# Kernel optimization log

Measured on AMD Instinct MI355X. Metric: run time of the kernel, lower is better.

Reference implementation:

```python
import jax, jax.numpy as jnp
import numpy as np

N_QUBITS = 10
Q_DEPTH = 6
MAX_LAYERS = 15
DIM = 2 ** N_QUBITS
INV_SQRT2 = 0.7071067811865476

# PennyLane ordering: wire 0 is the most-significant bit of the state index.
# All gates (H, RY, CNOT) are real, so the state stays real float32.

def _split(state, wire):
    a = 2 ** wire
    b = 2 ** (N_QUBITS - wire - 1)
    return state.reshape(-1, a, 2, b)

def apply_h(state, wire):
    s = _split(state, wire)
    s0, s1 = s[:, :, 0], s[:, :, 1]
    out = jnp.stack([(s0 + s1) * INV_SQRT2, (s0 - s1) * INV_SQRT2], axis=2)
    return out.reshape(-1, DIM)

def apply_ry(state, theta, wire):
    # theta: scalar (shared weight) or (B,) per-sample angle
    c = jnp.cos(theta * 0.5).reshape(-1, 1, 1)
    sn = jnp.sin(theta * 0.5).reshape(-1, 1, 1)
    s = _split(state, wire)
    s0, s1 = s[:, :, 0], s[:, :, 1]
    out = jnp.stack([c * s0 - sn * s1, sn * s0 + c * s1], axis=2)
    return out.reshape(-1, DIM)

def apply_cnot(state, ctrl):
    # CNOT on adjacent wires [ctrl, ctrl+1]
    a = 2 ** ctrl
    b = 2 ** (N_QUBITS - ctrl - 2)
    s = state.reshape(-1, a, 2, 2, b)
    out = jnp.stack([s[:, :, 0], s[:, :, 1, ::-1]], axis=2)
    return out.reshape(-1, DIM)

def expval_z(state):
    # <Z_j> = P(qubit j = 0) - P(qubit j = 1)
    zs = []
    for w in range(N_QUBITS):
        s = _split(state, w)
        p = s * s
        zs.append(jnp.sum(p[:, :, 0], axis=(1, 2)) - jnp.sum(p[:, :, 1], axis=(1, 2)))
    return jnp.stack(zs, axis=1)  # (B, n_qubits)

def simulate(q_in, q_params):
    B = q_in.shape[0]
    qw = q_params.reshape(MAX_LAYERS, N_QUBITS)
    state = jnp.zeros((B, DIM), q_in.dtype).at[:, 0].set(1.0)
    for w in range(N_QUBITS):
        state = apply_h(state, w)
    for w in range(N_QUBITS):
        state = apply_ry(state, q_in[:, w], w)
    for k in range(Q_DEPTH):
        for i in range(0, N_QUBITS - 1, 2):
            state = apply_cnot(state, i)
        for i in range(1, N_QUBITS - 1, 2):
            state = apply_cnot(state, i)
        for w in range(N_QUBITS):
            state = apply_ry(state, qw[k + 1, w], w)
    return expval_z(state)

def setup_inputs() -> dict:
    key = jax.random.key(0)
    k1, k2, k3, k4, k5 = jax.random.split(key, 5)
    B, D_IN, N_CLASSES = 8192, 512, 2
    return {
        "input_features": jax.random.normal(k1, (B, D_IN), jnp.float32),
        "W_red": jax.random.normal(k2, (N_QUBITS, D_IN), jnp.float32) * 0.04,
        "b_red": jnp.zeros((N_QUBITS,), jnp.float32),
        "q_params": 0.01 * jax.random.normal(k3, (MAX_LAYERS * N_QUBITS,), jnp.float32),
        "W_post": jax.random.normal(k4, (N_CLASSES, N_QUBITS), jnp.float32) * 0.3,
        "b_post": jax.random.normal(k5, (N_CLASSES,), jnp.float32) * 0.01,
    }

def reference(input_features, W_red, b_red, q_params, W_post, b_post):
    pre_out = input_features @ W_red.T + b_red           # (B, n_qubits)
    q_in = jnp.tanh(pre_out) * (np.pi / 2.0)             # angles in (-pi/2, pi/2)
    q_out = simulate(q_in, q_params)                     # (B, n_qubits) PauliZ expvals
    return q_out @ W_post.T + b_post                     # (B, n_classes)
```

## Files before the change

kernel.cpp:

```cpp
#include <hip/hip_runtime.h>
#include <math.h>

#define QDEPTH 6

typedef _Float16 h2 __attribute__((ext_vector_type(2)));

__device__ __forceinline__ int   h2i(h2 v)  { return __builtin_bit_cast(int, v); }
__device__ __forceinline__ h2    ih2(int v) { return __builtin_bit_cast(h2, v); }

__device__ __forceinline__ h2 cvt_pk(float a, float b) {
  return __builtin_bit_cast(h2, __builtin_amdgcn_cvt_pkrtz(a, b));
}

__device__ __forceinline__ h2 bper(int addr, h2 v) {
  return ih2(__builtin_amdgcn_ds_bpermute(addr, h2i(v)));
}

template<int CTRL>
__device__ __forceinline__ h2 dpph(h2 v) {
  int i = h2i(v);
  return ih2(__builtin_amdgcn_update_dpp(i, i, CTRL, 0xF, 0xF, true));
}

template<int CTRL>
__device__ __forceinline__ float dpp_add0(float v) {
  int i = __float_as_int(v);
  int r = __builtin_amdgcn_update_dpp(0, i, CTRL, 0xF, 0xF, false);
  return v + __int_as_float(r);
}

__device__ __forceinline__ float wave_sum(float v) {
  v = dpp_add0<0x111>(v);
  v = dpp_add0<0x112>(v);
  v = dpp_add0<0x114>(v);
  v = dpp_add0<0x118>(v);
  v = dpp_add0<0x142>(v);
  v = dpp_add0<0x143>(v);
  return v;
}

__device__ __forceinline__ float bcast63(float v) {
  return __int_as_float(__builtin_amdgcn_readlane(__float_as_int(v), 63));
}

__device__ __forceinline__ void pl32s(int& a, int& b) {
  asm("v_permlane32_swap_b32 %0, %1" : "+v"(a), "+v"(b));
}
__device__ __forceinline__ void pl16s(int& a, int& b) {
  asm("v_permlane16_swap_b32 %0, %1" : "+v"(a), "+v"(b));
}

__global__ void setup_kernel(const float* __restrict__ qp, unsigned* __restrict__ cb) {
  int t = threadIdx.x;
  if (t >= 60) return;
  int k = t / 10, w = t % 10;
  float ang = qp[(k + 1) * 10 + w] * 0.5f;
  float c = __cosf(ang), s = __sinf(ang);
  unsigned* p = cb + k * 32 + ((w < 9) ? w * 3 : 27);
  h2 cc = { (_Float16)c, (_Float16)c };
  if (w < 9) {
    h2 ss = { (_Float16)s,  (_Float16)s };
    h2 ns = { (_Float16)(-s), (_Float16)(-s) };
    p[0] = __builtin_bit_cast(unsigned, cc);
    p[1] = __builtin_bit_cast(unsigned, ss);
    p[2] = __builtin_bit_cast(unsigned, ns);
  } else {
    h2 ms = { (_Float16)(-s), (_Float16)s };
    p[0] = __builtin_bit_cast(unsigned, cc);
    p[1] = __builtin_bit_cast(unsigned, ms);
  }
}

__global__ void __launch_bounds__(256) qnet_kernel(
    const float* __restrict__ inp,
    const float* __restrict__ Wred,
    const float* __restrict__ bred,
    const unsigned* __restrict__ cb,
    const float* __restrict__ Wpost,
    const float* __restrict__ bpost,
    float* __restrict__ out,
    int B) {
  __shared__ unsigned sco[QDEPTH * 29];
  int tt = threadIdx.x;
  if (tt < QDEPTH * 29) sco[tt] = cb[(tt / 29) * 32 + (tt % 29)];
  __syncthreads();

  int tid  = blockIdx.x * 256 + threadIdx.x;
  int wv   = tid >> 6;
  int lane = tid & 63;

  int o = lane ^ (((lane >> 4) & 1) << 3) ^ (((lane >> 2) & 1) << 1);
  int psrc = o ^ (((o >> 5) & 1) << 4) ^ (((o >> 3) & 1) << 2) ^ ((o >> 1) & 1);
  int addrP  = psrc << 2;
  int addrX4 = (lane ^ 4) << 2;
  bool cb1 = lane & 1;

  const float4* row4 = (const float4*)(inp + (size_t)wv * 512);
  float4 a0 = row4[lane], a1 = row4[lane + 64];
  float th[10];
#pragma unroll
  for (int q = 0; q < 10; ++q) {
    const float4* w4 = (const float4*)(Wred + q * 512);
    float4 b0 = w4[lane], b1 = w4[lane + 64];
    float t = a0.x * b0.x + a0.y * b0.y + a0.z * b0.z + a0.w * b0.w;
    t += a1.x * b1.x + a1.y * b1.y + a1.z * b1.z + a1.w * b1.w;
    th[q] = t;
  }

  float g0[10], g1[10];
#pragma unroll
  for (int q = 0; q < 10; ++q) {
    float tot = bcast63(wave_sum(th[q])) + bred[q];
    float xc = fminf(fmaxf(tot, -15.f), 15.f);
    float u = __expf(2.f * xc);
    float tanhv = (u - 1.f) * __builtin_amdgcn_rcpf(u + 1.f);
    float t = tanhv * 0.78539816339744831f;
    float c = __cosf(t), s = __sinf(t);
    g0[q] = (c - s) * 0.70710678118654752f;
    g1[q] = (c + s) * 0.70710678118654752f;
  }
  float lf = 1.f;
#pragma unroll
  for (int w = 0; w < 6; ++w)
    lf *= ((lane >> (5 - w)) & 1) ? g1[w] : g0[w];
  float f67v[4];
#pragma unroll
  for (int j = 0; j < 4; ++j)
    f67v[j] = ((j & 2) ? g1[6] : g0[6]) * ((j & 1) ? g1[7] : g0[7]);
  float F89x[2], F89y[2];
  F89x[0] = g0[8] * g0[9]; F89y[0] = g0[8] * g1[9];
  F89x[1] = g1[8] * g0[9]; F89y[1] = g1[8] * g1[9];

  h2 x[8];
#pragma unroll
  for (int i = 0; i < 8; ++i) {
    float m = lf * f67v[i >> 1];
    x[i] = cvt_pk(m * F89x[i & 1], m * F89y[i & 1]);
  }

  for (int k = 0; k < QDEPTH; ++k) {
    const unsigned* L = sco + k * 29;
    h2 cc9 = ih2(L[27]), ms9 = ih2(L[28]);
    h2 cc6 = ih2(L[18]), ss6 = ih2(L[19]), ns6 = ih2(L[20]);
    h2 cc7 = ih2(L[21]), ss7 = ih2(L[22]), ns7 = ih2(L[23]);
    h2 cc8 = ih2(L[24]), ss8 = ih2(L[25]), ns8 = ih2(L[26]);
    h2 cc0 = ih2(L[0]),  ss0 = ih2(L[1]),  ns0 = ih2(L[2]);
    h2 cc1 = ih2(L[3]),  ss1 = ih2(L[4]),  ns1 = ih2(L[5]);
    h2 cc2 = ih2(L[6]),  ss2 = ih2(L[7]),  ns2 = ih2(L[8]);
    h2 cc3 = ih2(L[9]),  ss3 = ih2(L[10]), ns3 = ih2(L[11]);
    h2 cc4 = ih2(L[12]), ss4 = ih2(L[13]), ns4 = ih2(L[14]);
    h2 cc5 = ih2(L[15]), ss5 = ih2(L[16]), ns5 = ih2(L[17]);

#pragma unroll
    for (int i = 0; i < 8; ++i) x[i] = bper(addrP, x[i]);
    { h2 t = x[4]; x[4] = x[6]; x[6] = t; t = x[5]; x[5] = x[7]; x[7] = t; }
    { h2 t = x[2]; x[2] = x[3]; x[3] = t; t = x[6]; x[6] = x[7]; x[7] = t; }

#pragma unroll
    for (int i = 0; i < 8; ++i) {
      h2 t = __builtin_shufflevector(x[i], x[i], 1, 0);
      bool flg = (i == 1 || i == 2 || i == 5 || i == 6);
      x[i] = flg ? (h2)(t * cc9 + x[i] * ms9) : (h2)(x[i] * cc9 + t * ms9);
    }

    {
      h2 AA = cb1 ? ns6 : cc6;
      h2 BB = cb1 ? cc6 : ns6;
      h2 CC = cb1 ? cc6 : ss6;
      h2 DD = cb1 ? ss6 : cc6;
#pragma unroll
      for (int i = 0; i < 4; ++i) {
        h2 u = x[i], w = x[i + 4];
        x[i]     = u * AA + w * BB;
        x[i + 4] = u * CC + w * DD;
      }
    }
#pragma unroll
    for (int i = 0; i < 8; ++i) if (!(i & 2)) {
      h2 u = x[i], w = x[i | 2];
      x[i]     = u * cc7 + w * ns7;
      x[i | 2] = w * cc7 + u * ss7;
    }
#pragma unroll
    for (int i = 0; i < 8; ++i) if (!(i & 1)) {
      h2 u = x[i], w = x[i | 1];
      x[i]     = u * cc8 + w * ns8;
      x[i | 1] = w * cc8 + u * ss8;
    }

#pragma unroll
    for (int j = 0; j < 4; ++j) {
      int a = h2i(x[2 * j]), b = h2i(x[2 * j + 1]);
      pl32s(a, b);
      h2 u = ih2(a), v = ih2(b);
      h2 nu = u * cc0 + v * ns0;
      h2 nv = v * cc0 + u * ss0;
      int na = h2i(nu), nb = h2i(nv);
      pl32s(na, nb);
      x[2 * j] = ih2(na); x[2 * j + 1] = ih2(nb);
    }
#pragma unroll
    for (int j = 0; j < 4; ++j) {
      int a = h2i(x[2 * j]), b = h2i(x[2 * j + 1]);
      pl16s(a, b);
      h2 u = ih2(a), v = ih2(b);
      h2 nu = u * cc1 + v * ns1;
      h2 nv = v * cc1 + u * ss1;
      int na = h2i(nu), nb = h2i(nv);
      pl16s(na, nb);
      x[2 * j] = ih2(na); x[2 * j + 1] = ih2(nb);
    }
    {
      h2 gg = (lane & 8) ? ss2 : ns2;
#pragma unroll
      for (int i = 0; i < 8; ++i) {
        h2 p = dpph<0x128>(x[i]);
        x[i] = x[i] * cc2 + p * gg;
      }
    }
    {
      h2 gg = (lane & 4) ? ss3 : ns3;
#pragma unroll
      for (int i = 0; i < 8; ++i) {
        h2 p = bper(addrX4, x[i]);
        x[i] = x[i] * cc3 + p * gg;
      }
    }
    {
      h2 gg = (lane & 2) ? ss4 : ns4;
#pragma unroll
      for (int i = 0; i < 8; ++i) {
        h2 p = dpph<0x4E>(x[i]);
        x[i] = x[i] * cc4 + p * gg;
      }
    }
    {
      h2 gg = (lane & 1) ? ss5 : ns5;
#pragma unroll
      for (int i = 0; i < 8; ++i) {
        h2 p = dpph<0xB1>(x[i]);
        x[i] = x[i] * cc5 + p * gg;
      }
    }
  }

  float q[8], d9 = 0.f;
#pragma unroll
  for (int i = 0; i < 8; ++i) {
    float lo = (float)x[i].x, hi = (float)x[i].y;
    float a2 = lo * lo, b2 = hi * hi;
    q[i] = a2 + b2;
    d9 += a2 - b2;
  }
  float A = q[0] + q[1], Bq = q[2] + q[3], C = q[4] + q[5], D = q[6] + q[7];
  float S  = (A + Bq) + (C + D);
  float z6 = (A + Bq) - (C + D);
  float z7 = (A - Bq) + (C - D);
  float E = q[0] - q[1], F = q[2] - q[3], G = q[4] - q[5], H = q[6] - q[7];
  float z8 = (E + F) + (G + H);
  float z9 = d9;

  float A0 = 0.f, A1 = 0.f;
#pragma unroll
  for (int w = 0; w < 6; ++w) {
    bool b = (lane >> (5 - w)) & 1;
    A0 += b ? -Wpost[w] : Wpost[w];
    A1 += b ? -Wpost[10 + w] : Wpost[10 + w];
  }
  float o0 = A0 * S + Wpost[6] * z6 + Wpost[7] * z7 + Wpost[8] * z8 + Wpost[9] * z9;
  float o1 = A1 * S + Wpost[16] * z6 + Wpost[17] * z7 + Wpost[18] * z8 + Wpost[19] * z9;
  o0 = wave_sum(o0);
  o1 = wave_sum(o1);
  if (lane == 63) {
    float2 ov = { o0 + bpost[0], o1 + bpost[1] };
    *(float2*)(out + 2 * (size_t)wv) = ov;
  }
}

extern "C" void kernel_launch(void* const* d_in, const int* in_sizes, int n_in,
                              void* d_out, int out_size, void* d_ws, size_t ws_size,
                              hipStream_t stream) {
  const float* inp   = (const float*)d_in[0];
  const float* Wred  = (const float*)d_in[1];
  const float* bred  = (const float*)d_in[2];
  const float* qp    = (const float*)d_in[3];
  const float* Wpost = (const float*)d_in[4];
  const float* bpost = (const float*)d_in[5];
  float* out = (float*)d_out;
  unsigned* cbuf = (unsigned*)d_ws;

  int B = in_sizes[0] / 512;
  setup_kernel<<<1, 64, 0, stream>>>(qp, cbuf);
  int blocks = (B * 64) / 256;
  qnet_kernel<<<blocks, 256, 0, stream>>>(inp, Wred, bred, cbuf, Wpost, bpost, out, B);
}
```

Measured before the change: 99.23 us.

## Process two samples per wavefront and fold setup kernel into main kernel

```diff
diff --git a/kernel.cpp b/kernel.cpp
--- a/kernel.cpp
+++ b/kernel.cpp
@@ -7,6 +7,7 @@
 
 __device__ __forceinline__ int   h2i(h2 v)  { return __builtin_bit_cast(int, v); }
 __device__ __forceinline__ h2    ih2(int v) { return __builtin_bit_cast(h2, v); }
+__device__ __forceinline__ unsigned h2u(h2 v) { return __builtin_bit_cast(unsigned, v); }
 
 __device__ __forceinline__ h2 cvt_pk(float a, float b) {
   return __builtin_bit_cast(h2, __builtin_amdgcn_cvt_pkrtz(a, b));
@@ -50,39 +51,33 @@
   asm("v_permlane16_swap_b32 %0, %1" : "+v"(a), "+v"(b));
 }
 
-__global__ void setup_kernel(const float* __restrict__ qp, unsigned* __restrict__ cb) {
-  int t = threadIdx.x;
-  if (t >= 60) return;
-  int k = t / 10, w = t % 10;
-  float ang = qp[(k + 1) * 10 + w] * 0.5f;
-  float c = __cosf(ang), s = __sinf(ang);
-  unsigned* p = cb + k * 32 + ((w < 9) ? w * 3 : 27);
-  h2 cc = { (_Float16)c, (_Float16)c };
-  if (w < 9) {
-    h2 ss = { (_Float16)s,  (_Float16)s };
-    h2 ns = { (_Float16)(-s), (_Float16)(-s) };
-    p[0] = __builtin_bit_cast(unsigned, cc);
-    p[1] = __builtin_bit_cast(unsigned, ss);
-    p[2] = __builtin_bit_cast(unsigned, ns);
-  } else {
-    h2 ms = { (_Float16)(-s), (_Float16)s };
-    p[0] = __builtin_bit_cast(unsigned, cc);
-    p[1] = __builtin_bit_cast(unsigned, ms);
-  }
-}
-
 __global__ void __launch_bounds__(256) qnet_kernel(
     const float* __restrict__ inp,
     const float* __restrict__ Wred,
     const float* __restrict__ bred,
-    const unsigned* __restrict__ cb,
+    const float* __restrict__ qp,
     const float* __restrict__ Wpost,
     const float* __restrict__ bpost,
     float* __restrict__ out,
     int B) {
   __shared__ unsigned sco[QDEPTH * 29];
-  int tt = threadIdx.x;
-  if (tt < QDEPTH * 29) sco[tt] = cb[(tt / 29) * 32 + (tt % 29)];
+  {
+    int t = threadIdx.x;
+    if (t < 60) {
+      int k = t / 10, w = t % 10;
+      float ang = qp[(k + 1) * 10 + w] * 0.5f;
+      float c = __cosf(ang), s = __sinf(ang);
+      _Float16 ch = (_Float16)c, sh = (_Float16)s, nh = (_Float16)(-s);
+      if (w < 9) {
+        sco[k * 29 + w * 3 + 0] = h2u((h2){ch, ch});
+        sco[k * 29 + w * 3 + 1] = h2u((h2){sh, sh});
+        sco[k * 29 + w * 3 + 2] = h2u((h2){nh, nh});
+      } else {
+        sco[k * 29 + 27] = h2u((h2){ch, ch});
+        sco[k * 29 + 28] = h2u((h2){nh, sh});
+      }
+    }
+  }
   __syncthreads();
 
   int tid  = blockIdx.x * 256 + threadIdx.x;
@@ -95,185 +90,194 @@
   int addrX4 = (lane ^ 4) << 2;
   bool cb1 = lane & 1;
 
-  const float4* row4 = (const float4*)(inp + (size_t)wv * 512);
-  float4 a0 = row4[lane], a1 = row4[lane + 64];
-  float th[10];
+  const float4* rA = (const float4*)(inp + (size_t)(2 * wv) * 512);
+  const float4* rB = (const float4*)(inp + (size_t)(2 * wv + 1) * 512);
+  float4 A0 = rA[lane], A1 = rA[lane + 64];
+  float4 B0 = rB[lane], B1 = rB[lane + 64];
+  float thA[10], thB[10];
 #pragma unroll
   for (int q = 0; q < 10; ++q) {
     const float4* w4 = (const float4*)(Wred + q * 512);
-    float4 b0 = w4[lane], b1 = w4[lane + 64];
-    float t = a0.x * b0.x + a0.y * b0.y + a0.z * b0.z + a0.w * b0.w;
-    t += a1.x * b1.x + a1.y * b1.y + a1.z * b1.z + a1.w * b1.w;
-    th[q] = t;
-  }
-
-  float g0[10], g1[10];
-#pragma unroll
-  for (int q = 0; q < 10; ++q) {
-    float tot = bcast63(wave_sum(th[q])) + bred[q];
-    float xc = fminf(fmaxf(tot, -15.f), 15.f);
-    float u = __expf(2.f * xc);
-    float tanhv = (u - 1.f) * __builtin_amdgcn_rcpf(u + 1.f);
-    float t = tanhv * 0.78539816339744831f;
-    float c = __cosf(t), s = __sinf(t);
-    g0[q] = (c - s) * 0.70710678118654752f;
-    g1[q] = (c + s) * 0.70710678118654752f;
-  }
-  float lf = 1.f;
-#pragma unroll
-  for (int w = 0; w < 6; ++w)
-    lf *= ((lane >> (5 - w)) & 1) ? g1[w] : g0[w];
-  float f67v[4];
-#pragma unroll
-  for (int j = 0; j < 4; ++j)
-    f67v[j] = ((j & 2) ? g1[6] : g0[6]) * ((j & 1) ? g1[7] : g0[7]);
-  float F89x[2], F89y[2];
-  F89x[0] = g0[8] * g0[9]; F89y[0] = g0[8] * g1[9];
-  F89x[1] = g1[8] * g0[9]; F89y[1] = g1[8] * g1[9];
-
-  h2 x[8];
-#pragma unroll
-  for (int i = 0; i < 8; ++i) {
-    float m = lf * f67v[i >> 1];
-    x[i] = cvt_pk(m * F89x[i & 1], m * F89y[i & 1]);
-  }
-
+    float4 w0 = w4[lane], w1 = w4[lane + 64];
+    thA[q] = A0.x * w0.x + A0.y * w0.y + A0.z * w0.z + A0.w * w0.w
+           + A1.x * w1.x + A1.y * w1.y + A1.z * w1.z + A1.w * w1.w;
+    thB[q] = B0.x * w0.x + B0.y * w0.y + B0.z * w0.z + B0.w * w0.w
+           + B1.x * w1.x + B1.y * w1.y + B1.z * w1.z + B1.w * w1.w;
+  }
+
+  h2 x[16];
+
+#pragma unroll
+  for (int e = 0; e < 2; ++e) {
+    float g0[10], g1[10];
+#pragma unroll
+    for (int q = 0; q < 10; ++q) {
+      float tot = bcast63(wave_sum(e ? thB[q] : thA[q])) + bred[q];
+      float xc = fminf(fmaxf(tot, -15.f), 15.f);
+      float u = __expf(2.f * xc);
+      float tanhv = (u - 1.f) * __builtin_amdgcn_rcpf(u + 1.f);
+      float t = tanhv * 0.78539816339744831f;
+      float c = __cosf(t), s = __sinf(t);
+      g0[q] = (c - s) * 0.70710678118654752f;
+      g1[q] = (c + s) * 0.70710678118654752f;
+    }
+    float lf = 1.f;
+#pragma unroll
+    for (int w = 0; w < 6; ++w)
+      lf *= ((lane >> (5 - w)) & 1) ? g1[w] : g0[w];
+    float f67v[4];
+#pragma unroll
+    for (int j = 0; j < 4; ++j)
+      f67v[j] = ((j & 2) ? g1[6] : g0[6]) * ((j & 1) ? g1[7] : g0[7]);
+    float F89x[2], F89y[2];
+    F89x[0] = g0[8] * g0[9]; F89y[0] = g0[8] * g1[9];
+    F89x[1] = g1[8] * g0[9]; F89y[1] = g1[8] * g1[9];
+#pragma unroll
+    for (int i = 0; i < 8; ++i) {
+      float m = lf * f67v[i >> 1];
+      x[e * 8 + i] = cvt_pk(m * F89x[i & 1], m * F89y[i & 1]);
+    }
+  }
+
+#pragma unroll
   for (int k = 0; k < QDEPTH; ++k) {
     const unsigned* L = sco + k * 29;
-    h2 cc9 = ih2(L[27]), ms9 = ih2(L[28]);
-    h2 cc6 = ih2(L[18]), ss6 = ih2(L[19]), ns6 = ih2(L[20]);
-    h2 cc7 = ih2(L[21]), ss7 = ih2(L[22]), ns7 = ih2(L[23]);
-    h2 cc8 = ih2(L[24]), ss8 = ih2(L[25]), ns8 = ih2(L[26]);
-    h2 cc0 = ih2(L[0]),  ss0 = ih2(L[1]),  ns0 = ih2(L[2]);
-    h2 cc1 = ih2(L[3]),  ss1 = ih2(L[4]),  ns1 = ih2(L[5]);
-    h2 cc2 = ih2(L[6]),  ss2 = ih2(L[7]),  ns2 = ih2(L[8]);
-    h2 cc3 = ih2(L[9]),  ss3 = ih2(L[10]), ns3 = ih2(L[11]);
-    h2 cc4 = ih2(L[12]), ss4 = ih2(L[13]), ns4 = ih2(L[14]);
-    h2 cc5 = ih2(L[15]), ss5 = ih2(L[16]), ns5 = ih2(L[17]);
-
-#pragma unroll
-    for (int i = 0; i < 8; ++i) x[i] = bper(addrP, x[i]);
-    { h2 t = x[4]; x[4] = x[6]; x[6] = t; t = x[5]; x[5] = x[7]; x[7] = t; }
-    { h2 t = x[2]; x[2] = x[3]; x[3] = t; t = x[6]; x[6] = x[7]; x[7] = t; }
-
-#pragma unroll
-    for (int i = 0; i < 8; ++i) {
-      h2 t = __builtin_shufflevector(x[i], x[i], 1, 0);
-      bool flg = (i == 1 || i == 2 || i == 5 || i == 6);
-      x[i] = flg ? (h2)(t * cc9 + x[i] * ms9) : (h2)(x[i] * cc9 + t * ms9);
-    }
-
-    {
+
+#pragma unroll
+    for (int i = 0; i < 16; ++i) x[i] = bper(addrP, x[i]);
+#pragma unroll
+    for (int e = 0; e < 16; e += 8) {
+      h2 t = x[e + 4]; x[e + 4] = x[e + 6]; x[e + 6] = t;
+      t = x[e + 5]; x[e + 5] = x[e + 7]; x[e + 7] = t;
+    }
+#pragma unroll
+    for (int e = 0; e < 16; e += 8) {
+      h2 t = x[e + 2]; x[e + 2] = x[e + 3]; x[e + 3] = t;
+      t = x[e + 6]; x[e + 6] = x[e + 7]; x[e + 7] = t;
+    }
+
+    { h2 cc9 = ih2(L[27]), ms9 = ih2(L[28]);
+#pragma unroll
+      for (int i = 0; i < 16; ++i) {
+        h2 t = __builtin_shufflevector(x[i], x[i], 1, 0);
+        int m = i & 7;
+        bool flg = (m == 1 || m == 2 || m == 5 || m == 6);
+        x[i] = flg ? (h2)(t * cc9 + x[i] * ms9) : (h2)(x[i] * cc9 + t * ms9);
+      } }
+
+    { h2 cc6 = ih2(L[18]), ss6 = ih2(L[19]), ns6 = ih2(L[20]);
       h2 AA = cb1 ? ns6 : cc6;
       h2 BB = cb1 ? cc6 : ns6;
       h2 CC = cb1 ? cc6 : ss6;
       h2 DD = cb1 ? ss6 : cc6;
 #pragma unroll
-      for (int i = 0; i < 4; ++i) {
+      for (int i = 0; i < 16; ++i) if (!(i & 4)) {
         h2 u = x[i], w = x[i + 4];
         x[i]     = u * AA + w * BB;
         x[i + 4] = u * CC + w * DD;
-      }
-    }
-#pragma unroll
-    for (int i = 0; i < 8; ++i) if (!(i & 2)) {
-      h2 u = x[i], w = x[i | 2];
-      x[i]     = u * cc7 + w * ns7;
-      x[i | 2] = w * cc7 + u * ss7;
-    }
-#pragma unroll
-    for (int i = 0; i < 8; ++i) if (!(i & 1)) {
-      h2 u = x[i], w = x[i | 1];
-      x[i]     = u * cc8 + w * ns8;
-      x[i | 1] = w * cc8 + u * ss8;
-    }
-
-#pragma unroll
-    for (int j = 0; j < 4; ++j) {
-      int a = h2i(x[2 * j]), b = h2i(x[2 * j + 1]);
-      pl32s(a, b);
-      h2 u = ih2(a), v = ih2(b);
-      h2 nu = u * cc0 + v * ns0;
-      h2 nv = v * cc0 + u * ss0;
-      int na = h2i(nu), nb = h2i(nv);
-      pl32s(na, nb);
-      x[2 * j] = ih2(na); x[2 * j + 1] = ih2(nb);
-    }
-#pragma unroll
-    for (int j = 0; j < 4; ++j) {
-      int a = h2i(x[2 * j]), b = h2i(x[2 * j + 1]);
-      pl16s(a, b);
-      h2 u = ih2(a), v = ih2(b);
-      h2 nu = u * cc1 + v * ns1;
-      h2 nv = v * cc1 + u * ss1;
-      int na = h2i(nu), nb = h2i(nv);
-      pl16s(na, nb);
-      x[2 * j] = ih2(na); x[2 * j + 1] = ih2(nb);
-    }
-    {
+      } }
+    { h2 cc7 = ih2(L[21]), ss7 = ih2(L[22]), ns7 = ih2(L[23]);
+#pragma unroll
+      for (int i = 0; i < 16; ++i) if (!(i & 2)) {
+        h2 u = x[i], w = x[i | 2];
+        x[i]     = u * cc7 + w * ns7;
+        x[i | 2] = w * cc7 + u * ss7;
+      } }
+    { h2 cc8 = ih2(L[24]), ss8 = ih2(L[25]), ns8 = ih2(L[26]);
+#pragma unroll
+      for (int i = 0; i < 16; ++i) if (!(i & 1)) {
+        h2 u = x[i], w = x[i | 1];
+        x[i]     = u * cc8 + w * ns8;
+        x[i | 1] = w * cc8 + u * ss8;
+      } }
+
+    { h2 cc0 = ih2(L[0]), ss0 = ih2(L[1]), ns0 = ih2(L[2]);
+#pragma unroll
+      for (int j = 0; j < 8; ++j) {
+        int a = h2i(x[2 * j]), b = h2i(x[2 * j + 1]);
+        pl32s(a, b);
+        h2 u = ih2(a), v = ih2(b);
+        h2 nu = u * cc0 + v * ns0;
+        h2 nv = v * cc0 + u * ss0;
+        int na = h2i(nu), nb = h2i(nv);
+        pl32s(na, nb);
+        x[2 * j] = ih2(na); x[2 * j + 1] = ih2(nb);
+      } }
+    { h2 cc1 = ih2(L[3]), ss1 = ih2(L[4]), ns1 = ih2(L[5]);
+#pragma unroll
+      for (int j = 0; j < 8; ++j) {
+        int a = h2i(x[2 * j]), b = h2i(x[2 * j + 1]);
+        pl16s(a, b);
+        h2 u = ih2(a), v = ih2(b);
+        h2 nu = u * cc1 + v * ns1;
+        h2 nv = v * cc1 + u * ss1;
+        int na = h2i(nu), nb = h2i(nv);
+        pl16s(na, nb);
+        x[2 * j] = ih2(na); x[2 * j + 1] = ih2(nb);
+      } }
+    { h2 cc2 = ih2(L[6]), ss2 = ih2(L[7]), ns2 = ih2(L[8]);
       h2 gg = (lane & 8) ? ss2 : ns2;
 #pragma unroll
-      for (int i = 0; i < 8; ++i) {
+      for (int i = 0; i < 16; ++i) {
         h2 p = dpph<0x128>(x[i]);
         x[i] = x[i] * cc2 + p * gg;
-      }
-    }
-    {
+      } }
+    { h2 cc3 = ih2(L[9]), ss3 = ih2(L[10]), ns3 = ih2(L[11]);
       h2 gg = (lane & 4) ? ss3 : ns3;
 #pragma unroll
-      for (int i = 0; i < 8; ++i) {
+      for (int i = 0; i < 16; ++i) {
         h2 p = bper(addrX4, x[i]);
         x[i] = x[i] * cc3 + p * gg;
-      }
-    }
-    {
+      } }
+    { h2 cc4 = ih2(L[12]), ss4 = ih2(L[13]), ns4 = ih2(L[14]);
       h2 gg = (lane & 2) ? ss4 : ns4;
 #pragma unroll
-      for (int i = 0; i < 8; ++i) {
+      for (int i = 0; i < 16; ++i) {
         h2 p = dpph<0x4E>(x[i]);
         x[i] = x[i] * cc4 + p * gg;
-      }
-    }
-    {
+      } }
+    { h2 cc5 = ih2(L[15]), ss5 = ih2(L[16]), ns5 = ih2(L[17]);
       h2 gg = (lane & 1) ? ss5 : ns5;
 #pragma unroll
-      for (int i = 0; i < 8; ++i) {
+      for (int i = 0; i < 16; ++i) {
         h2 p = dpph<0xB1>(x[i]);
         x[i] = x[i] * cc5 + p * gg;
-      }
-    }
-  }
-
-  float q[8], d9 = 0.f;
-#pragma unroll
-  for (int i = 0; i < 8; ++i) {
-    float lo = (float)x[i].x, hi = (float)x[i].y;
-    float a2 = lo * lo, b2 = hi * hi;
-    q[i] = a2 + b2;
-    d9 += a2 - b2;
-  }
-  float A = q[0] + q[1], Bq = q[2] + q[3], C = q[4] + q[5], D = q[6] + q[7];
-  float S  = (A + Bq) + (C + D);
-  float z6 = (A + Bq) - (C + D);
-  float z7 = (A - Bq) + (C - D);
-  float E = q[0] - q[1], F = q[2] - q[3], G = q[4] - q[5], H = q[6] - q[7];
-  float z8 = (E + F) + (G + H);
-  float z9 = d9;
-
-  float A0 = 0.f, A1 = 0.f;
+      } }
+  }
+
+  float A0w = 0.f, A1w = 0.f;
 #pragma unroll
   for (int w = 0; w < 6; ++w) {
     bool b = (lane >> (5 - w)) & 1;
-    A0 += b ? -Wpost[w] : Wpost[w];
-    A1 += b ? -Wpost[10 + w] : Wpost[10 + w];
-  }
-  float o0 = A0 * S + Wpost[6] * z6 + Wpost[7] * z7 + Wpost[8] * z8 + Wpost[9] * z9;
-  float o1 = A1 * S + Wpost[16] * z6 + Wpost[17] * z7 + Wpost[18] * z8 + Wpost[19] * z9;
-  o0 = wave_sum(o0);
-  o1 = wave_sum(o1);
+    A0w += b ? -Wpost[w] : Wpost[w];
+    A1w += b ? -Wpost[10 + w] : Wpost[10 + w];
+  }
+  float oo[4];
+#pragma unroll
+  for (int e = 0; e < 2; ++e) {
+    float q[8], d9 = 0.f;
+#pragma unroll
+    for (int i = 0; i < 8; ++i) {
+      float lo = (float)x[e * 8 + i].x, hi = (float)x[e * 8 + i].y;
+      float a2 = lo * lo, b2 = hi * hi;
+      q[i] = a2 + b2;
+      d9 += a2 - b2;
+    }
+    float A = q[0] + q[1], Bq = q[2] + q[3], C = q[4] + q[5], D = q[6] + q[7];
+    float S  = (A + Bq) + (C + D);
+    float z6 = (A + Bq) - (C + D);
+    float z7 = (A - Bq) + (C - D);
+    float E = q[0] - q[1], F = q[2] - q[3], G = q[4] - q[5], H = q[6] - q[7];
+    float z8 = (E + F) + (G + H);
+    float o0 = A0w * S + Wpost[6] * z6 + Wpost[7] * z7 + Wpost[8] * z8 + Wpost[9] * d9;
+    float o1 = A1w * S + Wpost[16] * z6 + Wpost[17] * z7 + Wpost[18] * z8 + Wpost[19] * d9;
+    oo[2 * e]     = wave_sum(o0);
+    oo[2 * e + 1] = wave_sum(o1);
+  }
   if (lane == 63) {
-    float2 ov = { o0 + bpost[0], o1 + bpost[1] };
-    *(float2*)(out + 2 * (size_t)wv) = ov;
+    float4 ov = { oo[0] + bpost[0], oo[1] + bpost[1],
+                  oo[2] + bpost[0], oo[3] + bpost[1] };
+    *(float4*)(out + 4 * (size_t)wv) = ov;
   }
 }
 
@@ -287,10 +291,8 @@
   const float* Wpost = (const float*)d_in[4];
   const float* bpost = (const float*)d_in[5];
   float* out = (float*)d_out;
-  unsigned* cbuf = (unsigned*)d_ws;
 
   int B = in_sizes[0] / 512;
-  setup_kernel<<<1, 64, 0, stream>>>(qp, cbuf);
-  int blocks = (B * 64) / 256;
-  qnet_kernel<<<blocks, 256, 0, stream>>>(inp, Wred, bred, cbuf, Wpost, bpost, out, B);
-}
+  int blocks = (B * 32) / 256;
+  qnet_kernel<<<blocks, 256, 0, stream>>>(inp, Wred, bred, qp, Wpost, bpost, out, B);
+}
```

New measurement: 99.02 us. About the same (-0.2%).
